# Kernel tuning notes

Measured on AMD Instinct MI355X. Metric: run time of the kernel, lower is better.

Reference implementation:

```python
import jax, jax.numpy as jnp
import numpy as np

B, D, H = 8192, 1024, 1024

def setup_inputs() -> dict:
    key = jax.random.key(0)
    ks = jax.random.split(key, 7)
    s_x = 1.0 / np.sqrt(D)
    s_h = 1.0 / np.sqrt(H)
    return {
        "e_t": jax.random.normal(ks[0], (B, D), jnp.float32),
        "h_prev": jax.random.normal(ks[1], (B, H), jnp.float32),
        "c_prev": jax.random.normal(ks[2], (B, H), jnp.float32),
        # gates concatenated in order (f, i, o, c), each block of size H
        "W_x": jax.random.uniform(ks[3], (4 * H, D), jnp.float32, -s_x, s_x),
        "b_x": jax.random.uniform(ks[4], (4 * H,), jnp.float32, -s_x, s_x),
        "W_h": jax.random.uniform(ks[5], (4 * H, H), jnp.float32, -s_h, s_h),
        "b_h": jax.random.uniform(ks[6], (4 * H,), jnp.float32, -s_h, s_h),
        "b_extra": jnp.zeros((4 * H,), jnp.float32),  # the b_f/b_i/b_o/b_c Parameters
    }

def reference(e_t, h_prev, c_prev, W_x, b_x, W_h, b_h, b_extra):
    # two fused GEMMs: [B,D]@[D,4H] and [B,H]@[H,4H]
    z = (jnp.einsum('bd,gd->bg', e_t, W_x)
         + jnp.einsum('bh,gh->bg', h_prev, W_h)
         + b_x + b_h + b_extra)  # [B, 4H]
    zf, zi, zo, zc = jnp.split(z, 4, axis=-1)
    g_t = jax.nn.sigmoid(zf)   # forget gate
    p_t = jax.nn.sigmoid(zi)   # input gate
    q_t = jax.nn.sigmoid(zo)   # output gate
    m_t_hat = jnp.tanh(zc)     # candidate cell
    c_t = g_t * c_prev + p_t * m_t_hat
    h_t = q_t * jnp.tanh(c_t)
    return (h_t, c_t)
```

## Files before the change

### kernel.cpp

```cpp
#include <hip/hip_runtime.h>
#include <stdint.h>

#define B_ROWS 8192
#define DH     1024
#define KTOT   2048
#define NTOT   4096

typedef __attribute__((ext_vector_type(8))) __bf16 bf16x8;
typedef __attribute__((ext_vector_type(4))) float  f32x4;

__device__ __forceinline__ unsigned short f2bf(float f) {
    unsigned int u = __float_as_uint(f);
    u += 0x7FFFu + ((u >> 16) & 1u);
    return (unsigned short)(u >> 16);
}

__device__ __forceinline__ float fast_sigmoid(float x) {
    return 1.0f / (1.0f + __expf(-x));
}
__device__ __forceinline__ float fast_tanh(float x) {
    float e = __expf(fminf(-2.0f * x, 80.0f));
    return (1.0f - e) / (1.0f + e);
}
__device__ __forceinline__ float sel4(float g0, float g1, float g2, float g3, int u) {
    float r = g0;
    r = (u == 1) ? g1 : r;
    r = (u == 2) ? g2 : r;
    r = (u == 3) ? g3 : r;
    return r;
}

__global__ __launch_bounds__(256) void pack_act(const float* __restrict__ e_t,
                                                const float* __restrict__ h_prev,
                                                unsigned short* __restrict__ A_cat) {
    int idx8 = blockIdx.x * 256 + threadIdx.x;
    int row  = idx8 >> 8;
    int c8   = (idx8 & 255) << 3;
    const float* src = (c8 < DH) ? (e_t + (size_t)row * DH + c8)
                                 : (h_prev + (size_t)row * DH + (c8 - DH));
    float4 f0 = ((const float4*)src)[0];
    float4 f1 = ((const float4*)src)[1];
    uint4 o;
    o.x = (unsigned)f2bf(f0.x) | ((unsigned)f2bf(f0.y) << 16);
    o.y = (unsigned)f2bf(f0.z) | ((unsigned)f2bf(f0.w) << 16);
    o.z = (unsigned)f2bf(f1.x) | ((unsigned)f2bf(f1.y) << 16);
    o.w = (unsigned)f2bf(f1.z) | ((unsigned)f2bf(f1.w) << 16);
    *(uint4*)(A_cat + (size_t)idx8 * 8) = o;
}

__global__ __launch_bounds__(256) void pack_wts(const float* __restrict__ W_x,
                                                const float* __restrict__ W_h,
                                                unsigned short* __restrict__ W_cat) {
    int idx8 = blockIdx.x * 256 + threadIdx.x;
    int row  = idx8 >> 8;
    int c8   = (idx8 & 255) << 3;
    int h    = row >> 2;
    int gate = row & 3;
    int srow = gate * DH + h;
    const float* src = (c8 < DH) ? (W_x + (size_t)srow * DH + c8)
                                 : (W_h + (size_t)srow * DH + (c8 - DH));
    float4 f0 = ((const float4*)src)[0];
    float4 f1 = ((const float4*)src)[1];
    uint4 o;
    o.x = (unsigned)f2bf(f0.x) | ((unsigned)f2bf(f0.y) << 16);
    o.y = (unsigned)f2bf(f0.z) | ((unsigned)f2bf(f0.w) << 16);
    o.z = (unsigned)f2bf(f1.x) | ((unsigned)f2bf(f1.y) << 16);
    o.w = (unsigned)f2bf(f1.z) | ((unsigned)f2bf(f1.w) << 16);
    *(uint4*)(W_cat + (size_t)idx8 * 8) = o;
}

__global__ __launch_bounds__(256) void pack_bias(const float* __restrict__ b_x,
                                                 const float* __restrict__ b_h,
                                                 const float* __restrict__ b_e,
                                                 float* __restrict__ bias) {
    int gp = blockIdx.x * 256 + threadIdx.x;
    int h = gp >> 2, gate = gp & 3;
    int g = gate * DH + h;
    bias[gp] = b_x[g] + b_h[g] + b_e[g];
}

__global__ __launch_bounds__(256) void lstm_gemm(const unsigned short* __restrict__ A,
                                                 const unsigned short* __restrict__ Wc,
                                                 const float* __restrict__ bias,
                                                 const float* __restrict__ c_prev,
                                                 float* __restrict__ h_out,
                                                 float* __restrict__ c_out) {
    __shared__ __align__(16) unsigned char As[128 * 64 * 2];
    __shared__ __align__(16) unsigned char Bs[128 * 64 * 2];

    const int tid = threadIdx.x;
    const int w   = tid >> 6;
    const int l   = tid & 63;
    const int wm  = w >> 1, wn = w & 1;
    const int m0  = blockIdx.y * 128;
    const int n0  = blockIdx.x * 128;

    f32x4 acc[4][4];
#pragma unroll
    for (int i = 0; i < 4; ++i)
#pragma unroll
        for (int j = 0; j < 4; ++j) acc[i][j] = {0.f, 0.f, 0.f, 0.f};

    const int srow = w * 32 + (l >> 3);
    const int scol = (l & 7) * 8;
    const unsigned short* gA = A  + (size_t)(m0 + srow) * KTOT + scol;
    const unsigned short* gB = Wc + (size_t)(n0 + srow) * KTOT + scol;
    unsigned char* lA = As + w * 4096;
    unsigned char* lB = Bs + w * 4096;

    const int lane15 = l & 15;
    const int quad   = l >> 4;

    for (int kt = 0; kt < KTOT / 64; ++kt) {
#pragma unroll
        for (int i = 0; i < 4; ++i) {
            __builtin_amdgcn_global_load_lds(
                (const __attribute__((address_space(1))) void*)(gA + (size_t)(i * 8) * KTOT + kt * 64),
                (__attribute__((address_space(3))) void*)(lA + i * 1024), 16, 0, 0);
            __builtin_amdgcn_global_load_lds(
                (const __attribute__((address_space(1))) void*)(gB + (size_t)(i * 8) * KTOT + kt * 64),
                (__attribute__((address_space(3))) void*)(lB + i * 1024), 16, 0, 0);
        }
        __syncthreads();

#pragma unroll
        for (int ks = 0; ks < 2; ++ks) {
            bf16x8 af[4], bfr[4];
#pragma unroll
            for (int mi = 0; mi < 4; ++mi)
                af[mi] = *(const bf16x8*)(As + (wm * 64 + mi * 16 + lane15) * 128 + ks * 64 + quad * 16);
#pragma unroll
            for (int ni = 0; ni < 4; ++ni)
                bfr[ni] = *(const bf16x8*)(Bs + (wn * 64 + ni * 16 + lane15) * 128 + ks * 64 + quad * 16);
#pragma unroll
            for (int mi = 0; mi < 4; ++mi)
#pragma unroll
                for (int ni = 0; ni < 4; ++ni)
                    acc[mi][ni] = __builtin_amdgcn_mfma_f32_16x16x32_bf16(af[mi], bfr[ni], acc[mi][ni], 0, 0, 0);
        }
        __syncthreads();
    }

    float biasv[4];
#pragma unroll
    for (int nj = 0; nj < 4; ++nj)
        biasv[nj] = bias[n0 + wn * 64 + nj * 16 + lane15];

    const int u = (l >> 2) & 3;
    const int v = l & 3;
    const int src_base = (l & 0x30) | (v << 2);
    const int hbase = (n0 + wn * 64) >> 2;

#pragma unroll
    for (int mi = 0; mi < 4; ++mi) {
        const int m = m0 + wm * 64 + mi * 16 + quad * 4 + u;
#pragma unroll
        for (int nj = 0; nj < 4; ++nj) {
            f32x4 a = acc[mi][nj];
            float bb = biasv[nj];
            float a0 = a[0] + bb, a1 = a[1] + bb, a2 = a[2] + bb, a3 = a[3] + bb;

            float s0, s1, s2, s3;
            s0 = __shfl(a0, src_base | 0, 64); s1 = __shfl(a1, src_base | 0, 64);
            s2 = __shfl(a2, src_base | 0, 64); s3 = __shfl(a3, src_base | 0, 64);
            float zf = sel4(s0, s1, s2, s3, u);
            s0 = __shfl(a0, src_base | 1, 64); s1 = __shfl(a1, src_base | 1, 64);
            s2 = __shfl(a2, src_base | 1, 64); s3 = __shfl(a3, src_base | 1, 64);
            float zi = sel4(s0, s1, s2, s3, u);
            s0 = __shfl(a0, src_base | 2, 64); s1 = __shfl(a1, src_base | 2, 64);
            s2 = __shfl(a2, src_base | 2, 64); s3 = __shfl(a3, src_base | 2, 64);
            float zo = sel4(s0, s1, s2, s3, u);
            s0 = __shfl(a0, src_base | 3, 64); s1 = __shfl(a1, src_base | 3, 64);
            s2 = __shfl(a2, src_base | 3, 64); s3 = __shfl(a3, src_base | 3, 64);
            float zc = sel4(s0, s1, s2, s3, u);

            float gf = fast_sigmoid(zf);
            float gi = fast_sigmoid(zi);
            float go = fast_sigmoid(zo);
            float mh = fast_tanh(zc);

            const int h = hbase + nj * 4 + v;
            const size_t off = (size_t)m * DH + h;
            float cp = c_prev[off];
            float ct = gf * cp + gi * mh;
            float ht = go * fast_tanh(ct);
            h_out[off] = ht;
            c_out[off] = ct;
        }
    }
}

extern "C" void kernel_launch(void* const* d_in, const int* in_sizes, int n_in,
                              void* d_out, int out_size, void* d_ws, size_t ws_size,
                              hipStream_t stream) {
    const float* e_t     = (const float*)d_in[0];
    const float* h_prev  = (const float*)d_in[1];
    const float* c_prev  = (const float*)d_in[2];
    const float* W_x     = (const float*)d_in[3];
    const float* b_x     = (const float*)d_in[4];
    const float* W_h     = (const float*)d_in[5];
    const float* b_h     = (const float*)d_in[6];
    const float* b_extra = (const float*)d_in[7];

    float* h_out = (float*)d_out;
    float* c_out = h_out + (size_t)B_ROWS * DH;

    unsigned short* A_cat = (unsigned short*)d_ws;
    unsigned short* W_cat = (unsigned short*)((char*)d_ws + (size_t)B_ROWS * KTOT * 2);
    float*          bias  = (float*)((char*)d_ws + (size_t)B_ROWS * KTOT * 2 + (size_t)NTOT * KTOT * 2);

    pack_act <<<B_ROWS * KTOT / 8 / 256, 256, 0, stream>>>(e_t, h_prev, A_cat);
    pack_wts <<<NTOT   * KTOT / 8 / 256, 256, 0, stream>>>(W_x, W_h, W_cat);
    pack_bias<<<NTOT / 256,              256, 0, stream>>>(b_x, b_h, b_extra, bias);
    lstm_gemm<<<dim3(NTOT / 128, B_ROWS / 128), 256, 0, stream>>>(A_cat, W_cat, bias, c_prev, h_out, c_out);
}
```

Baseline: 354.6 us.

## XOR-swizzle LDS tiles and merge pack kernels into one launch

The GEMM now writes each 16-byte chunk of the A and B tiles to shared memory at an XOR-permuted column position, and reads fragments back with the matching swizzle. This is meant to remove the shared-memory bank conflicts caused by the 128-byte row stride when lanes read the same column across 16 rows. Separately, the three packing kernels (activations, weights, bias) are combined into one launch that picks its work from the block index, which removes two kernel launches. The swizzle must match exactly between the global-to-LDS copy and the fragment reads, or the results will be wrong.

After: 350.7 us. Within noise of the previous version (-1.1%).

```diff
diff --git a/kernel.cpp b/kernel.cpp
--- a/kernel.cpp
+++ b/kernel.cpp
@@ -30,53 +30,56 @@
     return r;
 }
 
-__global__ __launch_bounds__(256) void pack_act(const float* __restrict__ e_t,
+#define NBLK_A (B_ROWS)
+#define NBLK_W (NTOT)
+#define NBLK_BIAS (NTOT / 256)
+
+__global__ __launch_bounds__(256) void pack_all(const float* __restrict__ e_t,
                                                 const float* __restrict__ h_prev,
-                                                unsigned short* __restrict__ A_cat) {
-    int idx8 = blockIdx.x * 256 + threadIdx.x;
-    int row  = idx8 >> 8;
-    int c8   = (idx8 & 255) << 3;
-    const float* src = (c8 < DH) ? (e_t + (size_t)row * DH + c8)
-                                 : (h_prev + (size_t)row * DH + (c8 - DH));
-    float4 f0 = ((const float4*)src)[0];
-    float4 f1 = ((const float4*)src)[1];
-    uint4 o;
-    o.x = (unsigned)f2bf(f0.x) | ((unsigned)f2bf(f0.y) << 16);
-    o.y = (unsigned)f2bf(f0.z) | ((unsigned)f2bf(f0.w) << 16);
-    o.z = (unsigned)f2bf(f1.x) | ((unsigned)f2bf(f1.y) << 16);
-    o.w = (unsigned)f2bf(f1.z) | ((unsigned)f2bf(f1.w) << 16);
-    *(uint4*)(A_cat + (size_t)idx8 * 8) = o;
-}
-
-__global__ __launch_bounds__(256) void pack_wts(const float* __restrict__ W_x,
+                                                const float* __restrict__ W_x,
                                                 const float* __restrict__ W_h,
-                                                unsigned short* __restrict__ W_cat) {
-    int idx8 = blockIdx.x * 256 + threadIdx.x;
-    int row  = idx8 >> 8;
-    int c8   = (idx8 & 255) << 3;
-    int h    = row >> 2;
-    int gate = row & 3;
-    int srow = gate * DH + h;
-    const float* src = (c8 < DH) ? (W_x + (size_t)srow * DH + c8)
-                                 : (W_h + (size_t)srow * DH + (c8 - DH));
-    float4 f0 = ((const float4*)src)[0];
-    float4 f1 = ((const float4*)src)[1];
-    uint4 o;
-    o.x = (unsigned)f2bf(f0.x) | ((unsigned)f2bf(f0.y) << 16);
-    o.y = (unsigned)f2bf(f0.z) | ((unsigned)f2bf(f0.w) << 16);
-    o.z = (unsigned)f2bf(f1.x) | ((unsigned)f2bf(f1.y) << 16);
-    o.w = (unsigned)f2bf(f1.z) | ((unsigned)f2bf(f1.w) << 16);
-    *(uint4*)(W_cat + (size_t)idx8 * 8) = o;
-}
-
-__global__ __launch_bounds__(256) void pack_bias(const float* __restrict__ b_x,
-                                                 const float* __restrict__ b_h,
-                                                 const float* __restrict__ b_e,
-                                                 float* __restrict__ bias) {
-    int gp = blockIdx.x * 256 + threadIdx.x;
-    int h = gp >> 2, gate = gp & 3;
-    int g = gate * DH + h;
-    bias[gp] = b_x[g] + b_h[g] + b_e[g];
+                                                const float* __restrict__ b_x,
+                                                const float* __restrict__ b_h,
+                                                const float* __restrict__ b_e,
+                                                unsigned short* __restrict__ A_cat,
+                                                unsigned short* __restrict__ W_cat,
+                                                float* __restrict__ bias) {
+    const int blk = blockIdx.x;
+    const int t   = threadIdx.x;
+    if (blk < NBLK_A + NBLK_W) {
+        const float* src0;
+        unsigned short* dst;
+        int row;
+        if (blk < NBLK_A) {
+            row = blk;
+            src0 = nullptr;
+            dst = A_cat + (size_t)row * KTOT;
+            int c8 = t << 3;
+            src0 = (c8 < DH) ? (e_t + (size_t)row * DH + c8)
+                             : (h_prev + (size_t)row * DH + (c8 - DH));
+        } else {
+            row = blk - NBLK_A;
+            int h = row >> 2, gate = row & 3;
+            int srow = gate * DH + h;
+            dst = W_cat + (size_t)row * KTOT;
+            int c8 = t << 3;
+            src0 = (c8 < DH) ? (W_x + (size_t)srow * DH + c8)
+                             : (W_h + (size_t)srow * DH + (c8 - DH));
+        }
+        float4 f0 = ((const float4*)src0)[0];
+        float4 f1 = ((const float4*)src0)[1];
+        uint4 o;
+        o.x = (unsigned)f2bf(f0.x) | ((unsigned)f2bf(f0.y) << 16);
+        o.y = (unsigned)f2bf(f0.z) | ((unsigned)f2bf(f0.w) << 16);
+        o.z = (unsigned)f2bf(f1.x) | ((unsigned)f2bf(f1.y) << 16);
+        o.w = (unsigned)f2bf(f1.z) | ((unsigned)f2bf(f1.w) << 16);
+        *(uint4*)(dst + t * 8) = o;
+    } else {
+        int gp = (blk - NBLK_A - NBLK_W) * 256 + t;
+        int h = gp >> 2, gate = gp & 3;
+        int g = gate * DH + h;
+        bias[gp] = b_x[g] + b_h[g] + b_e[g];
+    }
 }
 
 __global__ __launch_bounds__(256) void lstm_gemm(const unsigned short* __restrict__ A,
@@ -102,7 +105,7 @@
         for (int j = 0; j < 4; ++j) acc[i][j] = {0.f, 0.f, 0.f, 0.f};
 
     const int srow = w * 32 + (l >> 3);
-    const int scol = (l & 7) * 8;
+    const int scol = (((l & 7) ^ ((l >> 3) & 7))) * 8;
     const unsigned short* gA = A  + (size_t)(m0 + srow) * KTOT + scol;
     const unsigned short* gB = Wc + (size_t)(n0 + srow) * KTOT + scol;
     unsigned char* lA = As + w * 4096;
@@ -110,6 +113,8 @@
 
     const int lane15 = l & 15;
     const int quad   = l >> 4;
+    const int xg0 = ((0 * 4 + quad) ^ (lane15 & 7)) * 16;
+    const int xg1 = ((1 * 4 + quad) ^ (lane15 & 7)) * 16;
 
     for (int kt = 0; kt < KTOT / 64; ++kt) {
 #pragma unroll
@@ -125,13 +130,14 @@
 
 #pragma unroll
         for (int ks = 0; ks < 2; ++ks) {
+            const int xg = ks ? xg1 : xg0;
             bf16x8 af[4], bfr[4];
 #pragma unroll
             for (int mi = 0; mi < 4; ++mi)
-                af[mi] = *(const bf16x8*)(As + (wm * 64 + mi * 16 + lane15) * 128 + ks * 64 + quad * 16);
+                af[mi] = *(const bf16x8*)(As + (wm * 64 + mi * 16 + lane15) * 128 + xg);
 #pragma unroll
             for (int ni = 0; ni < 4; ++ni)
-                bfr[ni] = *(const bf16x8*)(Bs + (wn * 64 + ni * 16 + lane15) * 128 + ks * 64 + quad * 16);
+                bfr[ni] = *(const bf16x8*)(Bs + (wn * 64 + ni * 16 + lane15) * 128 + xg);
 #pragma unroll
             for (int mi = 0; mi < 4; ++mi)
 #pragma unroll
@@ -209,8 +215,8 @@
     unsigned short* W_cat = (unsigned short*)((char*)d_ws + (size_t)B_ROWS * KTOT * 2);
     float*          bias  = (float*)((char*)d_ws + (size_t)B_ROWS * KTOT * 2 + (size_t)NTOT * KTOT * 2);
 
-    pack_act <<<B_ROWS * KTOT / 8 / 256, 256, 0, stream>>>(e_t, h_prev, A_cat);
-    pack_wts <<<NTOT   * KTOT / 8 / 256, 256, 0, stream>>>(W_x, W_h, W_cat);
-    pack_bias<<<NTOT / 256,              256, 0, stream>>>(b_x, b_h, b_extra, bias);
-    lstm_gemm<<<dim3(NTOT / 128, B_ROWS / 128), 256, 0, stream>>>(A_cat, W_cat, bias, c_prev, h_out, c_out);
-}
+    pack_all<<<NBLK_A + NBLK_W + NBLK_BIAS, 256, 0, stream>>>(
+        e_t, h_prev, W_x, W_h, b_x, b_h, b_extra, A_cat, W_cat, bias);
+    lstm_gemm<<<dim3(NTOT / 128, B_ROWS / 128), 256, 0, stream>>>(
+        A_cat, W_cat, bias, c_prev, h_out, c_out);
+}
```
